# Kernel optimization log

Hardware: AMD Instinct MI355X
Metric: run time of the kernel (lower is better)

The kernel has to match this reference:

```python
import jax, jax.numpy as jnp
import numpy as np

B, A, C, G = 8, 65536, 80, 16
TOPK = 50            # pre_anchor_topk
VAR0, VAR1 = 0.1, 0.2  # cfg['variance']
BBOX_T = 0.5
GAMMA = 2.0
ALPHA = 0.5
SL1_W, SL1_BETA = 0.75, 0.11


@jax.custom_vjp
def st_clip(x):
    # Clip.apply: clamp fwd, straight-through bwd
    return jnp.clip(x, 1e-12, None)

def _st_fwd(x):
    return jnp.clip(x, 1e-12, None), None

def _st_bwd(_, g):
    return (g,)

st_clip.defvjp(_st_fwd, _st_bwd)


def point_form(b):  # (cx,cy,w,h) -> (x1,y1,x2,y2)
    return jnp.concatenate([b[..., :2] - b[..., 2:] * 0.5,
                            b[..., :2] + b[..., 2:] * 0.5], axis=-1)


def decode(loc, priors):  # returns center form
    cxcy = priors[..., :2] + loc[..., :2] * VAR0 * priors[..., 2:]
    wh = priors[..., 2:] * jnp.exp(loc[..., 2:] * VAR1)
    return jnp.concatenate([cxcy, wh], axis=-1)


def encode(matched, priors):  # matched: point form, priors: center form
    g_cxcy = ((matched[..., :2] + matched[..., 2:]) * 0.5 - priors[..., :2]) / (VAR0 * priors[..., 2:])
    g_wh = jnp.log((matched[..., 2:] - matched[..., :2]) / priors[..., 2:]) / VAR1
    return jnp.concatenate([g_cxcy, g_wh], axis=-1)


def jaccard(a, b):  # a: [G,4], b: [A,4], point form -> [G,A] IoU
    lt = jnp.maximum(a[:, None, :2], b[None, :, :2])
    rb = jnp.minimum(a[:, None, 2:], b[None, :, 2:])
    wh = jnp.clip(rb - lt, 0.0, None)
    inter = wh[..., 0] * wh[..., 1]
    area_a = (a[:, 2] - a[:, 0]) * (a[:, 3] - a[:, 1])
    area_b = (b[:, 2] - b[:, 0]) * (b[:, 3] - b[:, 1])
    return inter / (area_a[:, None] + area_b[None, :] - inter)


def positive_bag_loss(logits):  # logits: [G, K], bag over K
    w = 1.0 / st_clip(1.0 - logits)
    w = w / jnp.sum(w, axis=1, keepdims=True)
    bag = jnp.sum(w * logits, axis=1)
    return -jnp.log(bag)


def setup_inputs() -> dict:
    key = jax.random.key(0)
    k1, k2, k3, k4, k5, k6 = jax.random.split(key, 6)
    box_regression = jax.random.normal(k1, (B, A, 4), jnp.float32) * 0.1
    cls_logits = jax.random.normal(k2, (B, A, C), jnp.float32) - 2.0
    a_cxcy = jax.random.uniform(k3, (A, 2), jnp.float32, 0.1, 0.9)
    a_wh = jax.random.uniform(k4, (A, 2), jnp.float32, 0.05, 0.3)
    anchors = jnp.concatenate([a_cxcy, a_wh], axis=-1)  # center form
    t_cxcy = jax.random.uniform(k5, (B, G, 2), jnp.float32, 0.2, 0.8)
    t_wh = jax.random.uniform(k6, (B, G, 2), jnp.float32, 0.05, 0.3)
    targets_boxes = jnp.concatenate([t_cxcy - t_wh * 0.5, t_cxcy + t_wh * 0.5], axis=-1)  # point form
    labels = jax.random.randint(jax.random.fold_in(key, 7), (B, G), 0, C)
    return {"box_regression": box_regression, "cls_logits": cls_logits,
            "anchors": anchors, "targets_boxes": targets_boxes, "labels": labels}


def _per_image(box_reg, cls_p, anchors, tboxes, tlabels):
    # ---- box_prob branch (torch: set_grad_enabled(False)) ----
    box_loc = point_form(decode(box_reg, anchors))
    iou = jaccard(tboxes, box_loc)                                  # [G, A]
    t2 = jnp.clip(jnp.max(iou, axis=1, keepdims=True), BBOX_T + 1e-12, None)
    obp = jnp.clip((iou - BBOX_T) / (t2 - BBOX_T), 0.0, 1.0)        # [G, A]
    # sparse per-class scatter + per-class max over objects == segment_max over labels
    seg = jax.ops.segment_max(obp, tlabels, num_segments=C)         # [C, A]
    image_box_prob = jax.lax.stop_gradient(jnp.maximum(seg, 0.0).T)  # [A, C]

    # ---- positive (bag) branch ----
    mqm = jaccard(tboxes, point_form(anchors))                      # [G, A]
    _, matched = jax.lax.top_k(mqm, TOPK)                           # [G, K]
    matched_cls_prob = cls_p[matched, tlabels[:, None]]             # [G, K]
    mot = encode(tboxes[:, None, :], anchors[matched])              # [G, K, 4]
    val = mot - box_reg[matched]
    sl1 = jnp.where(jnp.abs(val) < SL1_BETA,
                    0.5 / SL1_BETA * val * val,
                    jnp.abs(val) - 0.5 * SL1_BETA)
    reg_loss = SL1_W * jnp.sum(sl1, axis=-1)                        # [G, K]
    matched_box_prob = jnp.exp(-reg_loss)
    pos = positive_bag_loss(matched_cls_prob * matched_box_prob)    # [G]
    return pos, image_box_prob


def reference(box_regression, cls_logits, anchors, targets_boxes, labels):
    cls_prob = jax.nn.sigmoid(cls_logits)
    pos, box_prob = jax.vmap(_per_image, in_axes=(0, 0, None, 0, 0))(
        box_regression, cls_prob, anchors, targets_boxes, labels)
    n_pos = B * G
    positive_loss = jnp.sum(pos) / max(1, n_pos)
    x = cls_prob * (1.0 - box_prob)                                 # [B, A, C]
    negative_loss = jnp.sum(x ** GAMMA * -jnp.log(1.0 - x)) / max(1, n_pos * TOPK)
    return positive_loss * ALPHA, negative_loss * (1.0 - ALPHA)
```

## Files before the change

kernel.cpp:

```cpp
#include <hip/hip_runtime.h>
#include <hip/hip_bf16.h>
#include <math.h>

#define BB 8
#define AA 65536
#define CC 80
#define GG 16
#define KK 50
#define NBG (BB*GG)
#define CAP 2048
#define BINS 64
#define NCH 128
#define CHUNK (AA/NCH)
#define NIOU (NCH*BB)
#define NNEG 1024
#define NEGS   262144u
#define NPAIR1 13
#define NPAIR2 7
#define NEG0BASE (26u*NEGS)

#define OFF_ACC   0
#define OFF_T2    16
#define OFF_THR   528
#define OFF_GMASK 1040
#define OFF_CNT   3600
#define OFF_CCNT  4112
#define OFF_HIST  4128
#define HEAD_WORDS 9224
#define HEAD0 1032
#define OFF_CANDV 36896
#define OFF_CANDI 1085472
#define OFF_CLIST 2134048

__global__ void k_pre(unsigned* __restrict__ w, const int* __restrict__ labels,
                      unsigned* __restrict__ gmask){
    int tid=threadIdx.x;
    if (blockIdx.x==0){
        for (int i=tid; i<HEAD0; i+=256) w[i]=0u;
        __syncthreads();
        if (tid<NBG){
            int b=tid>>4; int c=labels[tid];
            atomicOr(&gmask[b*CC+c], 1u<<(tid&15));
        }
    } else {
        for (unsigned i=HEAD0+(blockIdx.x-1)*256u+tid; i<HEAD_WORDS; i+=63u*256u) w[i]=0u;
    }
}

#define NEGF4(v) { \
    float l0=v.x,l1=v.y,l2=v.z,l3=v.w; \
    float e0=__expf(l0), e1=__expf(l1), e2=__expf(l2), e3=__expf(l3); \
    float s0=e0*__builtin_amdgcn_rcpf(1.f+e0); \
    float s1=e1*__builtin_amdgcn_rcpf(1.f+e1); \
    float s2=e2*__builtin_amdgcn_rcpf(1.f+e2); \
    float s3=e3*__builtin_amdgcn_rcpf(1.f+e3); \
    fs+=s0*s0*__logf(1.f+e0); \
    fs+=s1*s1*__logf(1.f+e1); \
    fs+=s2*s2*__logf(1.f+e2); \
    fs+=s3*s3*__logf(1.f+e3); }

__global__ __launch_bounds__(256) void k_iou_neg(const float4* __restrict__ anc4,
        const float4* __restrict__ reg4, const float4* __restrict__ tgt4,
        const float4* __restrict__ lg4,
        unsigned* __restrict__ t2u, unsigned* __restrict__ ghist,
        int* __restrict__ ccnt, unsigned* __restrict__ clist,
        double* __restrict__ acc){
    __shared__ unsigned hist[GG][BINS];
    __shared__ float4 stb[GG];
    __shared__ float sarea[GG];
    __shared__ unsigned st2[GG];
    __shared__ unsigned lbuf[CHUNK];
    __shared__ int lcnt, lbase;
    __shared__ double wsum[4];
    int tid=threadIdx.x;
    int x=blockIdx.x;
    int id=(x>>4)*8+(x&7);

    if (((x>>3)&1)==0){
        double loc=0.0;
        unsigned i0=(unsigned)id*256u+(unsigned)tid;
        for (int gp=0; gp<NPAIR1; ++gp){
            float4 v0=lg4[i0];
            float4 v1=lg4[i0+NEGS];
            i0+=2u*NEGS;
            float fs=0.f;
            NEGF4(v0) NEGF4(v1)
            loc+=(double)fs;
        }
        for (int off=32; off; off>>=1) loc+=__shfl_down(loc,off);
        if ((tid&63)==0) wsum[tid>>6]=loc;
        __syncthreads();
        if (tid==0) atomicAdd(&acc[1],wsum[0]+wsum[1]+wsum[2]+wsum[3]);
        return;
    }

    int blk=id&(NCH-1), b=id>>7;
    for (int j=tid; j<GG*BINS; j+=256) ((unsigned*)hist)[j]=0u;
    if (tid<GG){
        float4 tb=tgt4[b*GG+tid];
        stb[tid]=tb;
        sarea[tid]=(tb.z-tb.x)*(tb.w-tb.y);
        st2[tid]=0u;
    }
    if (tid==0) lcnt=0;
    __syncthreads();
    float mx[GG];
    #pragma unroll
    for (int g=0; g<GG; ++g) mx[g]=0.f;
    int abase=blk*CHUNK+tid;
    for (int it=0; it<CHUNK/256; ++it){
        int a=abase+it*256;
        float4 an=anc4[a];
        float4 br=reg4[b*AA+a];
        float dcx=an.x+br.x*0.1f*an.z;
        float dcy=an.y+br.y*0.1f*an.w;
        float dw=an.z*__expf(br.z*0.2f);
        float dh=an.w*__expf(br.w*0.2f);
        float dx1=dcx-dw*0.5f, dy1=dcy-dh*0.5f, dx2=dcx+dw*0.5f, dy2=dcy+dh*0.5f;
        float dA=dw*dh;
        float ax1=an.x-an.z*0.5f, ay1=an.y-an.w*0.5f;
        float ax2=an.x+an.z*0.5f, ay2=an.y+an.w*0.5f;
        float aA=an.z*an.w;
        bool emit=false;
        #pragma unroll
        for (int g=0; g<GG; ++g){
            float4 tb=stb[g];
            float tA=sarea[g];
            {
                float lx=fmaxf(tb.x,dx1), ly=fmaxf(tb.y,dy1);
                float rx=fminf(tb.z,dx2), ry=fminf(tb.w,dy2);
                float w_=rx-lx, h_=ry-ly;
                if (w_>0.f && h_>0.f){
                    float inter=w_*h_;
                    float iou=inter/(tA+dA-inter);
                    mx[g]=fmaxf(mx[g],iou);
                    if (iou>0.5f) emit=true;
                }
            }
            {
                float lx=fmaxf(tb.x,ax1), ly=fmaxf(tb.y,ay1);
                float rx=fminf(tb.z,ax2), ry=fminf(tb.w,ay2);
                float w_=rx-lx, h_=ry-ly;
                if (w_>0.f && h_>0.f){
                    float inter=w_*h_;
                    float m=inter/(tA+aA-inter);
                    int bin=min(BINS-1,(int)(m*(float)BINS));
                    atomicAdd(&hist[g][bin],1u);
                }
            }
        }
        if (emit){
            int p=atomicAdd(&lcnt,1);
            lbuf[p]=(unsigned)a;
        }
    }
    #pragma unroll
    for (int g=0; g<GG; ++g){
        float v=mx[g];
        for (int off=32; off; off>>=1) v=fmaxf(v,__shfl_down(v,off));
        if ((tid&63)==0) atomicMax(&st2[g],__float_as_uint(v));
    }
    __syncthreads();
    if (tid<GG) atomicMax(&t2u[b*GG+tid],st2[tid]);
    if (tid==0 && lcnt>0) lbase=atomicAdd(ccnt,lcnt);
    __syncthreads();
    for (int j=tid; j<GG*BINS; j+=256){
        unsigned v=((unsigned*)hist)[j];
        if (v) atomicAdd(&ghist[b*GG*BINS+j],v);
    }
    unsigned bb=(unsigned)b<<16;
    for (int j=tid; j<lcnt; j+=256) clist[lbase+j]=bb|lbuf[j];

    {
        double loc=0.0;
        unsigned i0=NEG0BASE+(unsigned)id*256u+(unsigned)tid;
        for (int gp=0; gp<NPAIR2; ++gp){
            float4 v0=lg4[i0];
            float4 v1=lg4[i0+NEGS];
            i0+=2u*NEGS;
            float fs=0.f;
            NEGF4(v0) NEGF4(v1)
            loc+=(double)fs;
        }
        for (int off=32; off; off>>=1) loc+=__shfl_down(loc,off);
        if ((tid&63)==0) wsum[tid>>6]=loc;
        __syncthreads();
        if (tid==0) atomicAdd(&acc[1],wsum[0]+wsum[1]+wsum[2]+wsum[3]);
    }
}

__global__ __launch_bounds__(256) void k_candthr(const float4* __restrict__ anc4,
        const float4* __restrict__ tgt4, const unsigned* __restrict__ ghist,
        int* __restrict__ gcnt, float* __restrict__ candv, int* __restrict__ candi){
    __shared__ unsigned hist[GG][BINS];
    __shared__ float4 stb[GG];
    __shared__ float sarea[GG];
    __shared__ float sthr[GG];
    int tid=threadIdx.x, blk=blockIdx.x, b=blockIdx.y;
    int lane=tid&63, wv=tid>>6;
    for (int j=tid; j<GG*BINS; j+=256) ((unsigned*)hist)[j]=ghist[b*GG*BINS+j];
    if (tid<GG){
        float4 tb=tgt4[b*GG+tid];
        stb[tid]=tb;
        sarea[tid]=(tb.z-tb.x)*(tb.w-tb.y);
    }
    __syncthreads();
    #pragma unroll
    for (int gg=0; gg<4; ++gg){
        int g=wv*4+gg;
        unsigned v=hist[g][lane];
        #pragma unroll
        for (int off=1; off<64; off<<=1){
            unsigned o=__shfl_down(v,off);
            if (lane+off<64) v+=o;
        }
        unsigned long long mask=__ballot(v>=KK);
        int bs = mask ? (63-__clzll(mask)) : 0;
        if (lane==0) sthr[g]=(float)bs;
    }
    __syncthreads();
    int abase=blk*CHUNK+tid;
    for (int it=0; it<CHUNK/256; ++it){
        int a=abase+it*256;
        float4 an=anc4[a];
        float ax1=an.x-an.z*0.5f, ay1=an.y-an.w*0.5f;
        float ax2=an.x+an.z*0.5f, ay2=an.y+an.w*0.5f;
        float aA=an.z*an.w;
        #pragma unroll
        for (int g=0; g<GG; ++g){
            float4 tb=stb[g];
            float m=0.f;
            {
                float lx=fmaxf(tb.x,ax1), ly=fmaxf(tb.y,ay1);
                float rx=fminf(tb.z,ax2), ry=fminf(tb.w,ay2);
                float w_=rx-lx, h_=ry-ly;
                if (w_>0.f && h_>0.f){
                    float inter=w_*h_;
                    m=inter/(sarea[g]+aA-inter);
                }
            }
            bool push=(m>0.f && m*(float)BINS>=sthr[g]);
            unsigned long long msk=__ballot(push);
            if (msk){
                int bg=b*GG+g;
                int n=__popcll(msk);
                int ldr=__ffsll((long long)msk)-1;
                int base=0;
                if (lane==ldr) base=atomicAdd(&gcnt[bg],n);
                base=__shfl(base,ldr);
                if (push){
                    int p=base+(int)__popcll(msk&((1ull<<lane)-1ull));
                    if (p<CAP){ candv[bg*CAP+p]=m; candi[bg*CAP+p]=a; }
                }
            }
        }
    }
}

__global__ __launch_bounds__(256) void k_selcorr(const float4* __restrict__ anc4,
        const float4* __restrict__ reg4, const float4* __restrict__ tgt4,
        const float* __restrict__ logits, const int* __restrict__ labels,
        const int* __restrict__ gcnt, const float* __restrict__ candv,
        const int* __restrict__ candi, const unsigned* __restrict__ gmask,
        const float* __restrict__ t2f, const int* __restrict__ ccnt,
        const unsigned* __restrict__ clist, double* __restrict__ acc){
    __shared__ float cv[CAP];
    __shared__ int ci[CAP];
    __shared__ double wsum[4];
    int tid=threadIdx.x;
    int x=blockIdx.x;

    if (x>=NBG){
        int n=*ccnt;
        double loc=0.0;
        for (int i=(x-NBG)*256+tid; i<n; i+=256*256){
            unsigned key=clist[i];
            int b=key>>16, a=key&0xffff;
            float4 an=anc4[a];
            float4 br=reg4[b*AA+a];
            float dcx=an.x+br.x*0.1f*an.z;
            float dcy=an.y+br.y*0.1f*an.w;
            float dw=an.z*__expf(br.z*0.2f);
            float dh=an.w*__expf(br.w*0.2f);
            float dx1=dcx-dw*0.5f, dy1=dcy-dh*0.5f, dx2=dcx+dw*0.5f, dy2=dcy+dh*0.5f;
            float dA=dw*dh;
            float obp[GG];
            #pragma unroll
            for (int g=0; g<GG; ++g){
                float4 tb=tgt4[b*GG+g];
                float lx=fmaxf(tb.x,dx1), ly=fmaxf(tb.y,dy1);
                float rx=fminf(tb.z,dx2), ry=fminf(tb.w,dy2);
                float w_=fmaxf(rx-lx,0.f), h_=fmaxf(ry-ly,0.f);
                float inter=w_*h_;
                float tA=(tb.z-tb.x)*(tb.w-tb.y);
                float iou=inter/(tA+dA-inter);
                float d=t2f[b*GG+g]-0.5f;
                float inv=(d>0.f)?1.f/d:0.f;
                obp[g]=fminf(fmaxf((iou-0.5f)*inv,0.f),1.f);
            }
            for (int c=0; c<CC; ++c){
                unsigned m=gmask[b*CC+c];
                if (!m) continue;
                float bp=0.f;
                while (m){ unsigned g=(unsigned)__builtin_ctz(m); m&=m-1u; bp=fmaxf(bp,obp[g]); }
                if (bp<=0.f) continue;
                float lg=logits[((size_t)b*AA+(size_t)a)*CC+c];
                float e=__expf(lg);
                float s=e*__builtin_amdgcn_rcpf(1.f+e);
                float xx=s*(1.f-bp);
                float fx=xx*xx*(-__logf(fmaxf(1.f-xx,1e-12f)));
                float fs=s*s*__logf(1.f+e);
                loc+=(double)(fx-fs);
            }
        }
        for (int off=32; off; off>>=1) loc+=__shfl_down(loc,off);
        if ((tid&63)==0) wsum[tid>>6]=loc;
        __syncthreads();
        if (tid==0) atomicAdd(&acc[1],wsum[0]+wsum[1]+wsum[2]+wsum[3]);
        return;
    }

    int bg=x; int b=bg>>4;
    int cnt=gcnt[bg]; if (cnt>CAP) cnt=CAP;
    for (int j=tid; j<cnt; j+=256){ cv[j]=candv[bg*CAP+j]; ci[j]=candi[bg*CAP+j]; }
    __syncthreads();
    if (tid>=64) return;
    int lane=tid;
    int myA=-1;
    for (int k=0; k<KK; ++k){
        float bv=-1e30f; int bi=0x7fffffff; int bj=-1;
        for (int j=lane; j<cnt; j+=64){
            float v=cv[j]; int ii=ci[j];
            if (v>bv || (v==bv && ii<bi)){ bv=v; bi=ii; bj=j; }
        }
        for (int off=32; off; off>>=1){
            float ov=__shfl_down(bv,off); int oi=__shfl_down(bi,off); int oj=__shfl_down(bj,off);
            if (ov>bv || (ov==bv && oi<bi)){ bv=ov; bi=oi; bj=oj; }
        }
        int wj=__shfl(bj,0); int wi=__shfl(bi,0); float wv=__shfl(bv,0);
        if (wv>-1e29f){
            if (lane==(wj&63)) cv[wj]=-1e30f;
            if (lane==k) myA=wi;
        }
    }
    float p=0.f, u=0.f;
    if (lane<KK && myA>=0){
        float4 tb=tgt4[bg];
        int a=myA;
        float4 an=anc4[a];
        int lab=labels[bg];
        float lg=logits[((size_t)b*AA+(size_t)a)*CC+lab];
        float mcp=1.f/(1.f+expf(-lg));
        float gcx=((tb.x+tb.z)*0.5f-an.x)/(0.1f*an.z);
        float gcy=((tb.y+tb.w)*0.5f-an.y)/(0.1f*an.w);
        float gw=logf((tb.z-tb.x)/an.z)/0.2f;
        float gh=logf((tb.w-tb.y)/an.w)/0.2f;
        float4 br=reg4[b*AA+a];
        float v0=gcx-br.x, v1=gcy-br.y, v2=gw-br.z, v3=gh-br.w;
        float s=0.f;
        {float av=fabsf(v0); s+=(av<0.11f)?4.545454545454546f*v0*v0:av-0.055f;}
        {float av=fabsf(v1); s+=(av<0.11f)?4.545454545454546f*v1*v1:av-0.055f;}
        {float av=fabsf(v2); s+=(av<0.11f)?4.545454545454546f*v2*v2:av-0.055f;}
        {float av=fabsf(v3); s+=(av<0.11f)?4.545454545454546f*v3*v3:av-0.055f;}
        float mbp=expf(-(0.75f*s));
        p=mcp*mbp;
        u=1.f/fmaxf(1.f-p,1e-12f);
    }
    float su=u, sp=u*p;
    for (int off=32; off; off>>=1){ su+=__shfl_down(su,off); sp+=__shfl_down(sp,off); }
    if (lane==0) atomicAdd(&acc[0],(double)(-logf(sp/su)));
}

__global__ void k_fin(const double* __restrict__ acc, float* __restrict__ out){
    out[0]=(float)(0.5*acc[0]/128.0);
    out[1]=(float)(0.5*acc[1]/6400.0);
}

extern "C" void kernel_launch(void* const* d_in, const int* in_sizes, int n_in,
                              void* d_out, int out_size, void* d_ws, size_t ws_size,
                              hipStream_t stream){
    const float4* reg4=(const float4*)d_in[0];
    const float*  logits=(const float*)d_in[1];
    const float4* anc4=(const float4*)d_in[2];
    const float4* tgt4=(const float4*)d_in[3];
    const int*    labels=(const int*)d_in[4];
    char* ws=(char*)d_ws;
    double*   acc   =(double*)(ws+OFF_ACC);
    float*    t2f   =(float*)(ws+OFF_T2);
    unsigned* gmask =(unsigned*)(ws+OFF_GMASK);
    int*      gcnt  =(int*)(ws+OFF_CNT);
    int*      ccnt  =(int*)(ws+OFF_CCNT);
    unsigned* ghist =(unsigned*)(ws+OFF_HIST);
    float*    candv =(float*)(ws+OFF_CANDV);
    int*      candi =(int*)(ws+OFF_CANDI);
    unsigned* clist =(unsigned*)(ws+OFF_CLIST);

    k_pre<<<64,256,0,stream>>>((unsigned*)ws,labels,gmask);
    k_iou_neg<<<NNEG+NIOU,256,0,stream>>>(anc4,reg4,tgt4,(const float4*)logits,
                                          (unsigned*)t2f,ghist,ccnt,clist,acc);
    k_candthr<<<dim3(NCH,BB),256,0,stream>>>(anc4,tgt4,ghist,gcnt,candv,candi);
    k_selcorr<<<NBG+256,256,0,stream>>>(anc4,reg4,tgt4,logits,labels,gcnt,candv,candi,
                                        gmask,t2f,ccnt,clist,acc);
    k_fin<<<1,1,0,stream>>>(acc,(float*)d_out);
}
```

Baseline: 314.8 us.

## Parallelize top-k across four waves, spread negative-loss atomics, widen grids

Top-k selection in k_selcorr now runs in two stages. Each of the four waves picks its own top 50 from a quarter of the candidates, then one wave merges the 200 survivors, so the serial selection is no longer done by a single wave. Negative-loss partial sums are spread over 64 double accumulators, which k_fin sums, to reduce contention on one atomic address. The grids for k_candthr (256 chunks per image) and the correction branch of k_selcorr (1920 blocks) are also enlarged to add parallelism, at the cost of more blocks and more atomics on the candidate counters.

```diff
diff --git a/kernel.cpp b/kernel.cpp
--- a/kernel.cpp
+++ b/kernel.cpp
@@ -12,8 +12,11 @@
 #define BINS 64
 #define NCH 128
 #define CHUNK (AA/NCH)
+#define NCH2 256
+#define CHUNK2 (AA/NCH2)
 #define NIOU (NCH*BB)
 #define NNEG 1024
+#define NCORR 1920
 #define NEGS   262144u
 #define NPAIR1 13
 #define NPAIR2 7
@@ -21,7 +24,7 @@
 
 #define OFF_ACC   0
 #define OFF_T2    16
-#define OFF_THR   528
+#define OFF_ACCN  528
 #define OFF_GMASK 1040
 #define OFF_CNT   3600
 #define OFF_CCNT  4112
@@ -64,7 +67,7 @@
         const float4* __restrict__ lg4,
         unsigned* __restrict__ t2u, unsigned* __restrict__ ghist,
         int* __restrict__ ccnt, unsigned* __restrict__ clist,
-        double* __restrict__ acc){
+        double* __restrict__ accn){
     __shared__ unsigned hist[GG][BINS];
     __shared__ float4 stb[GG];
     __shared__ float sarea[GG];
@@ -90,7 +93,7 @@
         for (int off=32; off; off>>=1) loc+=__shfl_down(loc,off);
         if ((tid&63)==0) wsum[tid>>6]=loc;
         __syncthreads();
-        if (tid==0) atomicAdd(&acc[1],wsum[0]+wsum[1]+wsum[2]+wsum[3]);
+        if (tid==0) atomicAdd(&accn[x&63],wsum[0]+wsum[1]+wsum[2]+wsum[3]);
         return;
     }
 
@@ -185,7 +188,7 @@
         for (int off=32; off; off>>=1) loc+=__shfl_down(loc,off);
         if ((tid&63)==0) wsum[tid>>6]=loc;
         __syncthreads();
-        if (tid==0) atomicAdd(&acc[1],wsum[0]+wsum[1]+wsum[2]+wsum[3]);
+        if (tid==0) atomicAdd(&accn[x&63],wsum[0]+wsum[1]+wsum[2]+wsum[3]);
     }
 }
 
@@ -219,8 +222,8 @@
         if (lane==0) sthr[g]=(float)bs;
     }
     __syncthreads();
-    int abase=blk*CHUNK+tid;
-    for (int it=0; it<CHUNK/256; ++it){
+    int abase=blk*CHUNK2+tid;
+    for (int it=0; it<CHUNK2/256; ++it){
         int a=abase+it*256;
         float4 an=anc4[a];
         float ax1=an.x-an.z*0.5f, ay1=an.y-an.w*0.5f;
@@ -263,9 +266,12 @@
         const int* __restrict__ gcnt, const float* __restrict__ candv,
         const int* __restrict__ candi, const unsigned* __restrict__ gmask,
         const float* __restrict__ t2f, const int* __restrict__ ccnt,
-        const unsigned* __restrict__ clist, double* __restrict__ acc){
+        const unsigned* __restrict__ clist, double* __restrict__ acc,
+        double* __restrict__ accn){
     __shared__ float cv[CAP];
     __shared__ int ci[CAP];
+    __shared__ float sv[4*KK];
+    __shared__ int si[4*KK];
     __shared__ double wsum[4];
     int tid=threadIdx.x;
     int x=blockIdx.x;
@@ -273,7 +279,7 @@
     if (x>=NBG){
         int n=*ccnt;
         double loc=0.0;
-        for (int i=(x-NBG)*256+tid; i<n; i+=256*256){
+        for (int i=(x-NBG)*256+tid; i<n; i+=NCORR*256){
             unsigned key=clist[i];
             int b=key>>16, a=key&0xffff;
             float4 an=anc4[a];
@@ -316,7 +322,7 @@
         for (int off=32; off; off>>=1) loc+=__shfl_down(loc,off);
         if ((tid&63)==0) wsum[tid>>6]=loc;
         __syncthreads();
-        if (tid==0) atomicAdd(&acc[1],wsum[0]+wsum[1]+wsum[2]+wsum[3]);
+        if (tid==0) atomicAdd(&accn[x&63],wsum[0]+wsum[1]+wsum[2]+wsum[3]);
         return;
     }
 
@@ -324,24 +330,43 @@
     int cnt=gcnt[bg]; if (cnt>CAP) cnt=CAP;
     for (int j=tid; j<cnt; j+=256){ cv[j]=candv[bg*CAP+j]; ci[j]=candi[bg*CAP+j]; }
     __syncthreads();
+    int lane=tid&63, w=tid>>6;
+    {
+        int q=(cnt+3)>>2;
+        int lo=w*q; int hi=lo+q; if (hi>cnt) hi=cnt; if (lo>cnt) lo=cnt;
+        for (int k=0; k<KK; ++k){
+            float bv=-1e30f; int bi=0x7fffffff; int bj=-1;
+            for (int j=lo+lane; j<hi; j+=64){
+                float v=cv[j]; int ii=ci[j];
+                if (v>bv || (v==bv && ii<bi)){ bv=v; bi=ii; bj=j; }
+            }
+            for (int off=32; off; off>>=1){
+                float ov=__shfl_down(bv,off); int oi=__shfl_down(bi,off); int oj=__shfl_down(bj,off);
+                if (ov>bv || (ov==bv && oi<bi)){ bv=ov; bi=oi; bj=oj; }
+            }
+            float wvv=__shfl(bv,0); int wii=__shfl(bi,0); int wjj=__shfl(bj,0);
+            if (lane==0){
+                sv[w*KK+k]=wvv; si[w*KK+k]=wii;
+                if (wvv>-1e29f) cv[wjj]=-1e30f;
+            }
+        }
+    }
+    __syncthreads();
     if (tid>=64) return;
-    int lane=tid;
     int myA=-1;
     for (int k=0; k<KK; ++k){
         float bv=-1e30f; int bi=0x7fffffff; int bj=-1;
-        for (int j=lane; j<cnt; j+=64){
-            float v=cv[j]; int ii=ci[j];
-            if (v>bv || (v==bv && ii<bi)){ bv=v; bi=ii; bj=j; }
+        for (int e=lane; e<4*KK; e+=64){
+            float v=sv[e]; int ii=si[e];
+            if (v>bv || (v==bv && ii<bi)){ bv=v; bi=ii; bj=e; }
         }
         for (int off=32; off; off>>=1){
             float ov=__shfl_down(bv,off); int oi=__shfl_down(bi,off); int oj=__shfl_down(bj,off);
             if (ov>bv || (ov==bv && oi<bi)){ bv=ov; bi=oi; bj=oj; }
         }
-        int wj=__shfl(bj,0); int wi=__shfl(bi,0); float wv=__shfl(bv,0);
-        if (wv>-1e29f){
-            if (lane==(wj&63)) cv[wj]=-1e30f;
-            if (lane==k) myA=wi;
-        }
+        float wvv=__shfl(bv,0); int wii=__shfl(bi,0); int wjj=__shfl(bj,0);
+        if (lane==0 && wvv>-1e29f) sv[wjj]=-1e30f;
+        if (lane==k) myA=(wvv>-1e29f)?wii:-1;
     }
     float p=0.f, u=0.f;
     if (lane<KK && myA>=0){
@@ -371,9 +396,12 @@
     if (lane==0) atomicAdd(&acc[0],(double)(-logf(sp/su)));
 }
 
-__global__ void k_fin(const double* __restrict__ acc, float* __restrict__ out){
+__global__ void k_fin(const double* __restrict__ acc, const double* __restrict__ accn,
+                      float* __restrict__ out){
+    double s=acc[1];
+    for (int i=0; i<64; ++i) s+=accn[i];
     out[0]=(float)(0.5*acc[0]/128.0);
-    out[1]=(float)(0.5*acc[1]/6400.0);
+    out[1]=(float)(0.5*s/6400.0);
 }
 
 extern "C" void kernel_launch(void* const* d_in, const int* in_sizes, int n_in,
@@ -387,6 +415,7 @@
     char* ws=(char*)d_ws;
     double*   acc   =(double*)(ws+OFF_ACC);
     float*    t2f   =(float*)(ws+OFF_T2);
+    double*   accn  =(double*)(ws+OFF_ACCN);
     unsigned* gmask =(unsigned*)(ws+OFF_GMASK);
     int*      gcnt  =(int*)(ws+OFF_CNT);
     int*      ccnt  =(int*)(ws+OFF_CCNT);
@@ -397,9 +426,9 @@
 
     k_pre<<<64,256,0,stream>>>((unsigned*)ws,labels,gmask);
     k_iou_neg<<<NNEG+NIOU,256,0,stream>>>(anc4,reg4,tgt4,(const float4*)logits,
-                                          (unsigned*)t2f,ghist,ccnt,clist,acc);
-    k_candthr<<<dim3(NCH,BB),256,0,stream>>>(anc4,tgt4,ghist,gcnt,candv,candi);
-    k_selcorr<<<NBG+256,256,0,stream>>>(anc4,reg4,tgt4,logits,labels,gcnt,candv,candi,
-                                        gmask,t2f,ccnt,clist,acc);
-    k_fin<<<1,1,0,stream>>>(acc,(float*)d_out);
-}
+                                          (unsigned*)t2f,ghist,ccnt,clist,accn);
+    k_candthr<<<dim3(NCH2,BB),256,0,stream>>>(anc4,tgt4,ghist,gcnt,candv,candi);
+    k_selcorr<<<NBG+NCORR,256,0,stream>>>(anc4,reg4,tgt4,logits,labels,gcnt,candv,candi,
+                                          gmask,t2f,ccnt,clist,acc,accn);
+    k_fin<<<1,1,0,stream>>>(acc,accn,(float*)d_out);
+}
```

Measured after the change: 360.5 us. 1.14x slower.
